# Optimization experiments

Hardware: AMD Instinct MI355X
Metric: run time of the kernel (lower is better)

The kernel has to match this reference:

```python
import jax, jax.numpy as jnp
import numpy as np

N_NODES = 50000
N_EDGES = 600000
F_IN = 128
HID = 128
LN_EPS = 1e-5


def setup_inputs() -> dict:
    key = jax.random.key(0)
    ks = jax.random.split(key, 8)
    x = jax.random.normal(ks[0], (N_NODES, F_IN), dtype=jnp.float32)
    edge_index = jax.random.randint(ks[1], (2, N_EDGES), 0, N_NODES, dtype=jnp.int64)
    s1 = 1.0 / np.sqrt(F_IN)
    s2 = 1.0 / np.sqrt(HID)
    return {
        "x": x,
        "edge_index": edge_index,
        "W1": jax.random.normal(ks[2], (F_IN, HID), dtype=jnp.float32) * s1,
        "b1": jnp.zeros((HID,), dtype=jnp.float32),
        "g1": jnp.ones((HID,), dtype=jnp.float32),
        "be1": jnp.zeros((HID,), dtype=jnp.float32),
        "W2": jax.random.normal(ks[3], (HID, HID), dtype=jnp.float32) * s2,
        "b2": jnp.zeros((HID,), dtype=jnp.float32),
        "g2": jnp.ones((HID,), dtype=jnp.float32),
        "be2": jnp.zeros((HID,), dtype=jnp.float32),
    }


def _layer_norm(h, g, b):
    mu = jnp.mean(h, axis=-1, keepdims=True)
    var = jnp.mean(jnp.square(h - mu), axis=-1, keepdims=True)
    return (h - mu) * jax.lax.rsqrt(var + LN_EPS) * g + b


def reference(x, edge_index, W1, b1, g1, be1, W2, b2, g2, be2):
    n = x.shape[0]
    src, dst = edge_index[0], edge_index[1]
    # GCN symmetric normalization with self-loops: deg = in-degree(A) + 1
    deg = jax.ops.segment_sum(jnp.ones_like(src, dtype=x.dtype), dst, num_segments=n) + 1.0
    dinv = jax.lax.rsqrt(deg)                       # D^{-1/2}, [N]
    enorm = (dinv[src] * dinv[dst])[:, None]        # per-edge norm, [E,1]
    self_norm = (dinv * dinv)[:, None]              # self-loop norm,  [N,1]

    def gcn(h, W, b):
        h = h @ W                                   # [N,HID]
        agg = jax.ops.segment_sum(h[src] * enorm, dst, num_segments=n)
        return agg + h * self_norm + b

    h = jax.nn.relu(_layer_norm(gcn(x, W1, b1), g1, be1))
    h = jax.nn.relu(_layer_norm(gcn(h, W2, b2), g2, be2))
    return h  # dropout is identity in eval; LSTM evolution only runs in training
```

## Files before the change

kernel.cpp:

```cpp
#include <hip/hip_runtime.h>

#define N_NODES 50000
#define N_EDGES 600000
#define HID 128
#define LN_EPS 1e-5f
#define MAXDEG 64
#define NB_GEMM1 782
#define NB_PLACE 2344

typedef __attribute__((ext_vector_type(8))) short short8;
typedef __attribute__((ext_vector_type(4))) float f32x4;

__device__ inline float b2f(unsigned short u) {
    union { unsigned int i; float f; } v;
    v.i = ((unsigned int)u) << 16;
    return v.f;
}
__device__ inline unsigned short f2b(float f) {
    union { float f; unsigned int u; } v; v.f = f;
    unsigned int r = (v.u + 0x7FFFu + ((v.u >> 16) & 1u)) >> 16;
    return (unsigned short)r;
}

__global__ __launch_bounds__(256) void k_fused1(const float* __restrict__ x,
                                                const float* __restrict__ W1,
                                                const float* __restrict__ W2,
                                                const int* __restrict__ ei,
                                                int* __restrict__ cursor,
                                                int* __restrict__ esrc,
                                                unsigned short* __restrict__ WT2,
                                                unsigned short* __restrict__ hb) {
    const int tid = threadIdx.x;

    if (blockIdx.x >= NB_GEMM1) {
        const int bi = blockIdx.x - NB_GEMM1;
        const int e = bi * 256 + tid;
        if (e < N_EDGES) {
            const int d = ei[N_EDGES + e];
            const int pos = atomicAdd(&cursor[d], 1);
            if (pos < MAXDEG) esrc[d * MAXDEG + pos] = ei[e];
        }
        if (bi < 64) {
            const int i = bi * 256 + tid;
            const int k = i >> 7, n = i & 127;
            WT2[n * 128 + k] = f2b(W2[i]);
        }
        return;
    }

    __shared__ unsigned short wt[16384];
    {
        const float4* W4 = (const float4*)W1;
#pragma unroll
        for (int it = 0; it < 16; ++it) {
            const int i4 = tid + 256 * it;
            const float4 v = W4[i4];
            const int k  = (i4 * 4) >> 7;
            const int n0 = (i4 * 4) & 127;
            wt[(n0 + 0) * 128 + (k ^ (((n0 + 0) & 7) << 3))] = f2b(v.x);
            wt[(n0 + 1) * 128 + (k ^ (((n0 + 1) & 7) << 3))] = f2b(v.y);
            wt[(n0 + 2) * 128 + (k ^ (((n0 + 2) & 7) << 3))] = f2b(v.z);
            wt[(n0 + 3) * 128 + (k ^ (((n0 + 3) & 7) << 3))] = f2b(v.w);
        }
    }
    __syncthreads();

    const int lane = tid & 63;
    const int ln   = lane & 15;
    const int quad = lane >> 4;
    const int m0   = blockIdx.x * 64 + (tid >> 6) * 16;

    f32x4 acc[8];
#pragma unroll
    for (int t = 0; t < 8; ++t) acc[t] = (f32x4){0.f, 0.f, 0.f, 0.f};

    int arow = m0 + ln;
    if (arow >= N_NODES) arow = N_NODES - 1;
    const float* aptr = x + (size_t)arow * HID + quad * 8;

#pragma unroll
    for (int ks = 0; ks < 4; ++ks) {
        const float4 v0 = *(const float4*)(aptr + ks * 32);
        const float4 v1 = *(const float4*)(aptr + ks * 32 + 4);
        short8 a;
        a[0] = (short)f2b(v0.x); a[1] = (short)f2b(v0.y);
        a[2] = (short)f2b(v0.z); a[3] = (short)f2b(v0.w);
        a[4] = (short)f2b(v1.x); a[5] = (short)f2b(v1.y);
        a[6] = (short)f2b(v1.z); a[7] = (short)f2b(v1.w);
#pragma unroll
        for (int t = 0; t < 8; ++t) {
            const int n = t * 16 + ln;
            const short8 b = *(const short8*)&wt[n * 128 + ((quad * 8 + ks * 32) ^ ((n & 7) << 3))];
            acc[t] = __builtin_amdgcn_mfma_f32_16x16x32_bf16(a, b, acc[t], 0, 0, 0);
        }
    }

#pragma unroll
    for (int t = 0; t < 8; ++t) {
#pragma unroll
        for (int r = 0; r < 4; ++r) {
            const int row = m0 + quad * 4 + r;
            if (row < N_NODES) hb[(size_t)row * HID + t * 16 + ln] = f2b(acc[t][r]);
        }
    }
}

template <bool FUSE>
__device__ __forceinline__ void agg_body(const int* __restrict__ cursor,
                                         const int* __restrict__ esrc,
                                         const unsigned short* __restrict__ h,
                                         const float* __restrict__ bia,
                                         const float* __restrict__ g,
                                         const float* __restrict__ be,
                                         const unsigned short* __restrict__ WT2,
                                         unsigned short* __restrict__ hb2,
                                         float* __restrict__ outf) {
    __shared__ float pbuf[2048];
    const int tid  = threadIdx.x;
    const int wv   = tid >> 6;
    const int lane = tid & 63;
    const int grp  = lane >> 4;
    const int fl   = lane & 15;
    const int half = wv >> 2;
    const int r    = (wv & 3) * 4 + grp;
    const int row  = blockIdx.x * 16 + r;

    const int cntA  = cursor[row];
    const int cnt   = cntA < MAXDEG ? cntA : MAXDEG;
    const int ebase = row * MAXDEG;
    const int c0    = ((cnt + 7) >> 3) << 2;
    const int h0n   = c0 < cnt ? c0 : cnt;
    const int eb    = half ? ebase + h0n : ebase;
    const int ee    = half ? ebase + cnt : ebase + h0n;

    float acc[8];
#pragma unroll
    for (int j = 0; j < 8; ++j) acc[j] = 0.f;

    int e = eb;
    for (; e + 3 < ee; e += 4) {
        const int4 s4 = *(const int4*)(esrc + e);
        const float w0 = rsqrtf((float)cursor[s4.x] + 1.0f);
        const float w1 = rsqrtf((float)cursor[s4.y] + 1.0f);
        const float w2 = rsqrtf((float)cursor[s4.z] + 1.0f);
        const float w3 = rsqrtf((float)cursor[s4.w] + 1.0f);
        const short8 v0 = *(const short8*)(h + (size_t)s4.x * HID + 8 * fl);
        const short8 v1 = *(const short8*)(h + (size_t)s4.y * HID + 8 * fl);
        const short8 v2 = *(const short8*)(h + (size_t)s4.z * HID + 8 * fl);
        const short8 v3 = *(const short8*)(h + (size_t)s4.w * HID + 8 * fl);
#pragma unroll
        for (int j = 0; j < 8; ++j) {
            acc[j] = fmaf(w0, b2f((unsigned short)v0[j]), acc[j]);
            acc[j] = fmaf(w1, b2f((unsigned short)v1[j]), acc[j]);
            acc[j] = fmaf(w2, b2f((unsigned short)v2[j]), acc[j]);
            acc[j] = fmaf(w3, b2f((unsigned short)v3[j]), acc[j]);
        }
    }
    for (; e < ee; ++e) {
        const int sA = esrc[e];
        const float wA = rsqrtf((float)cursor[sA] + 1.0f);
        const short8 vA = *(const short8*)(h + (size_t)sA * HID + 8 * fl);
#pragma unroll
        for (int j = 0; j < 8; ++j)
            acc[j] = fmaf(wA, b2f((unsigned short)vA[j]), acc[j]);
    }

    if (half == 1) {
#pragma unroll
        for (int j = 0; j < 8; ++j) pbuf[r * 128 + 8 * fl + j] = acc[j];
    }
    __syncthreads();

    float o[8];
    if (half == 0) {
#pragma unroll
        for (int j = 0; j < 8; ++j) acc[j] += pbuf[r * 128 + 8 * fl + j];

        const float dd = rsqrtf((float)cntA + 1.0f);
        const float sn = dd * dd;
        const short8 hv = *(const short8*)(h + (size_t)row * HID + 8 * fl);
        const float4 b0 = *(const float4*)(bia + 8 * fl);
        const float4 b1 = *(const float4*)(bia + 8 * fl + 4);
        const float bb[8] = {b0.x, b0.y, b0.z, b0.w, b1.x, b1.y, b1.z, b1.w};

        float v[8], s = 0.f, ss = 0.f;
#pragma unroll
        for (int j = 0; j < 8; ++j) {
            v[j] = dd * acc[j] + b2f((unsigned short)hv[j]) * sn + bb[j];
            s += v[j];
            ss = fmaf(v[j], v[j], ss);
        }
#pragma unroll
        for (int off = 1; off <= 8; off <<= 1) {
            s  += __shfl_xor(s, off);
            ss += __shfl_xor(ss, off);
        }
        const float mu  = s * (1.0f / 128.0f);
        const float var = ss * (1.0f / 128.0f) - mu * mu;
        const float rs  = rsqrtf(var + LN_EPS);

        const float4 g0  = *(const float4*)(g + 8 * fl);
        const float4 g1  = *(const float4*)(g + 8 * fl + 4);
        const float4 e0v = *(const float4*)(be + 8 * fl);
        const float4 e1v = *(const float4*)(be + 8 * fl + 4);
        const float gg[8] = {g0.x, g0.y, g0.z, g0.w, g1.x, g1.y, g1.z, g1.w};
        const float ee2[8] = {e0v.x, e0v.y, e0v.z, e0v.w, e1v.x, e1v.y, e1v.z, e1v.w};
#pragma unroll
        for (int j = 0; j < 8; ++j)
            o[j] = fmaxf((v[j] - mu) * rs * gg[j] + ee2[j], 0.0f);
    }

    if constexpr (!FUSE) {
        if (half == 0) {
            float4 w0 = {o[0], o[1], o[2], o[3]};
            float4 w1 = {o[4], o[5], o[6], o[7]};
            *(float4*)(outf + (size_t)row * HID + 8 * fl) = w0;
            *(float4*)(outf + (size_t)row * HID + 8 * fl + 4) = w1;
        }
    } else {
        __syncthreads();
        unsigned short* tile = (unsigned short*)pbuf;
        if (half == 0) {
            short8 w;
#pragma unroll
            for (int j = 0; j < 8; ++j) w[j] = (short)f2b(o[j]);
            *(short8*)&tile[r * 128 + ((8 * fl) ^ ((r & 7) << 3))] = w;
        }
        __syncthreads();

        f32x4 c = (f32x4){0.f, 0.f, 0.f, 0.f};
        const int n0 = wv * 16 + fl;
#pragma unroll
        for (int ks = 0; ks < 4; ++ks) {
            const short8 a  = *(const short8*)&tile[fl * 128 + ((grp * 8 + ks * 32) ^ ((fl & 7) << 3))];
            const short8 bf = *(const short8*)(WT2 + (size_t)n0 * HID + grp * 8 + ks * 32);
            c = __builtin_amdgcn_mfma_f32_16x16x32_bf16(a, bf, c, 0, 0, 0);
        }
#pragma unroll
        for (int rr = 0; rr < 4; ++rr) {
            const int orow = blockIdx.x * 16 + grp * 4 + rr;
            hb2[(size_t)orow * HID + n0] = f2b(c[rr]);
        }
    }
}

__global__ __launch_bounds__(512, 4) void k_agg_fuse(const int* __restrict__ cursor,
                                                     const int* __restrict__ esrc,
                                                     const unsigned short* __restrict__ h,
                                                     const float* __restrict__ bia,
                                                     const float* __restrict__ g,
                                                     const float* __restrict__ be,
                                                     const unsigned short* __restrict__ WT2,
                                                     unsigned short* __restrict__ hb2) {
    agg_body<true>(cursor, esrc, h, bia, g, be, WT2, hb2, nullptr);
}

__global__ __launch_bounds__(512, 4) void k_agg_out(const int* __restrict__ cursor,
                                                    const int* __restrict__ esrc,
                                                    const unsigned short* __restrict__ h,
                                                    const float* __restrict__ bia,
                                                    const float* __restrict__ g,
                                                    const float* __restrict__ be,
                                                    float* __restrict__ outf) {
    agg_body<false>(cursor, esrc, h, bia, g, be, nullptr, nullptr, outf);
}

extern "C" void kernel_launch(void* const* d_in, const int* in_sizes, int n_in,
                              void* d_out, int out_size, void* d_ws, size_t ws_size,
                              hipStream_t stream) {
    (void)in_sizes; (void)n_in; (void)out_size; (void)ws_size;

    const float* x   = (const float*)d_in[0];
    const int*   ei  = (const int*)d_in[1];
    const float* W1  = (const float*)d_in[2];
    const float* b1  = (const float*)d_in[3];
    const float* g1  = (const float*)d_in[4];
    const float* be1 = (const float*)d_in[5];
    const float* W2  = (const float*)d_in[6];
    const float* b2  = (const float*)d_in[7];
    const float* g2  = (const float*)d_in[8];
    const float* be2 = (const float*)d_in[9];
    float* out = (float*)d_out;

    int* cursor = (int*)d_ws;
    int* esrc   = (int*)d_ws + 50016;
    unsigned short* WT2 = (unsigned short*)((int*)d_ws + 3250016);
    unsigned short* hb  = (unsigned short*)((int*)d_ws + 3258208);
    unsigned short* hb2 = (unsigned short*)((int*)d_ws + 6458208);

    hipMemsetAsync(cursor, 0, N_NODES * sizeof(int), stream);
    k_fused1<<<NB_GEMM1 + NB_PLACE, 256, 0, stream>>>(x, W1, W2, ei, cursor, esrc, WT2, hb);

    k_agg_fuse<<<N_NODES / 16, 512, 0, stream>>>(cursor, esrc, hb, b1, g1, be1, WT2, hb2);
    k_agg_out<<<N_NODES / 16, 512, 0, stream>>>(cursor, esrc, hb2, b2, g2, be2, out);
}
```

Before: 188.7 us.

## Pre-scale layer-2 features by source degree norm and move weight transposes to prep kernel

The layer-1 fused kernel now multiplies its GEMM2 output rows by the source-node D^{-1/2}. This lets the second aggregation sum raw features without per-edge cursor lookups and rsqrt, and fold the self-loop and destination scaling into a single dd factor. Weight bf16 transposes and the cursor zeroing move into a small prep kernel that replaces the memset. The GEMM1 blocks now read B fragments directly from global WT1 instead of building a swizzled LDS copy per block. The trade is an extra launch plus uncoalesced-ish global B loads in GEMM1, in exchange for removing redundant per-block transpose work and gather traffic in the second aggregation.

```diff
diff --git a/kernel.cpp b/kernel.cpp
--- a/kernel.cpp
+++ b/kernel.cpp
@@ -22,48 +22,41 @@
     return (unsigned short)r;
 }
 
+__global__ __launch_bounds__(256) void k_prep(const float* __restrict__ W1,
+                                              const float* __restrict__ W2,
+                                              unsigned short* __restrict__ WT1,
+                                              unsigned short* __restrict__ WT2,
+                                              int* __restrict__ cursor) {
+    const int bid = blockIdx.x, tid = threadIdx.x;
+    if (bid < 64) {
+        const int i = bid * 256 + tid;
+        WT1[(i & 127) * 128 + (i >> 7)] = f2b(W1[i]);
+    } else if (bid < 128) {
+        const int i = (bid - 64) * 256 + tid;
+        WT2[(i & 127) * 128 + (i >> 7)] = f2b(W2[i]);
+    } else {
+        const int i = (bid - 128) * 256 + tid;
+        if (i < N_NODES) cursor[i] = 0;
+    }
+}
+
 __global__ __launch_bounds__(256) void k_fused1(const float* __restrict__ x,
-                                                const float* __restrict__ W1,
-                                                const float* __restrict__ W2,
+                                                const unsigned short* __restrict__ WT1,
                                                 const int* __restrict__ ei,
                                                 int* __restrict__ cursor,
                                                 int* __restrict__ esrc,
-                                                unsigned short* __restrict__ WT2,
                                                 unsigned short* __restrict__ hb) {
     const int tid = threadIdx.x;
 
     if (blockIdx.x >= NB_GEMM1) {
-        const int bi = blockIdx.x - NB_GEMM1;
-        const int e = bi * 256 + tid;
+        const int e = (blockIdx.x - NB_GEMM1) * 256 + tid;
         if (e < N_EDGES) {
             const int d = ei[N_EDGES + e];
             const int pos = atomicAdd(&cursor[d], 1);
             if (pos < MAXDEG) esrc[d * MAXDEG + pos] = ei[e];
         }
-        if (bi < 64) {
-            const int i = bi * 256 + tid;
-            const int k = i >> 7, n = i & 127;
-            WT2[n * 128 + k] = f2b(W2[i]);
-        }
         return;
     }
-
-    __shared__ unsigned short wt[16384];
-    {
-        const float4* W4 = (const float4*)W1;
-#pragma unroll
-        for (int it = 0; it < 16; ++it) {
-            const int i4 = tid + 256 * it;
-            const float4 v = W4[i4];
-            const int k  = (i4 * 4) >> 7;
-            const int n0 = (i4 * 4) & 127;
-            wt[(n0 + 0) * 128 + (k ^ (((n0 + 0) & 7) << 3))] = f2b(v.x);
-            wt[(n0 + 1) * 128 + (k ^ (((n0 + 1) & 7) << 3))] = f2b(v.y);
-            wt[(n0 + 2) * 128 + (k ^ (((n0 + 2) & 7) << 3))] = f2b(v.z);
-            wt[(n0 + 3) * 128 + (k ^ (((n0 + 3) & 7) << 3))] = f2b(v.w);
-        }
-    }
-    __syncthreads();
 
     const int lane = tid & 63;
     const int ln   = lane & 15;
@@ -77,6 +70,7 @@
     int arow = m0 + ln;
     if (arow >= N_NODES) arow = N_NODES - 1;
     const float* aptr = x + (size_t)arow * HID + quad * 8;
+    const unsigned short* bptr = WT1 + (size_t)ln * HID + quad * 8;
 
 #pragma unroll
     for (int ks = 0; ks < 4; ++ks) {
@@ -89,8 +83,7 @@
         a[6] = (short)f2b(v1.z); a[7] = (short)f2b(v1.w);
 #pragma unroll
         for (int t = 0; t < 8; ++t) {
-            const int n = t * 16 + ln;
-            const short8 b = *(const short8*)&wt[n * 128 + ((quad * 8 + ks * 32) ^ ((n & 7) << 3))];
+            const short8 b = *(const short8*)(bptr + (size_t)t * 16 * HID + ks * 32);
             acc[t] = __builtin_amdgcn_mfma_f32_16x16x32_bf16(a, b, acc[t], 0, 0, 0);
         }
     }
@@ -140,26 +133,35 @@
     int e = eb;
     for (; e + 3 < ee; e += 4) {
         const int4 s4 = *(const int4*)(esrc + e);
-        const float w0 = rsqrtf((float)cursor[s4.x] + 1.0f);
-        const float w1 = rsqrtf((float)cursor[s4.y] + 1.0f);
-        const float w2 = rsqrtf((float)cursor[s4.z] + 1.0f);
-        const float w3 = rsqrtf((float)cursor[s4.w] + 1.0f);
         const short8 v0 = *(const short8*)(h + (size_t)s4.x * HID + 8 * fl);
         const short8 v1 = *(const short8*)(h + (size_t)s4.y * HID + 8 * fl);
         const short8 v2 = *(const short8*)(h + (size_t)s4.z * HID + 8 * fl);
         const short8 v3 = *(const short8*)(h + (size_t)s4.w * HID + 8 * fl);
-#pragma unroll
-        for (int j = 0; j < 8; ++j) {
-            acc[j] = fmaf(w0, b2f((unsigned short)v0[j]), acc[j]);
-            acc[j] = fmaf(w1, b2f((unsigned short)v1[j]), acc[j]);
-            acc[j] = fmaf(w2, b2f((unsigned short)v2[j]), acc[j]);
-            acc[j] = fmaf(w3, b2f((unsigned short)v3[j]), acc[j]);
+        if constexpr (FUSE) {
+            const float w0 = rsqrtf((float)cursor[s4.x] + 1.0f);
+            const float w1 = rsqrtf((float)cursor[s4.y] + 1.0f);
+            const float w2 = rsqrtf((float)cursor[s4.z] + 1.0f);
+            const float w3 = rsqrtf((float)cursor[s4.w] + 1.0f);
+#pragma unroll
+            for (int j = 0; j < 8; ++j) {
+                acc[j] = fmaf(w0, b2f((unsigned short)v0[j]), acc[j]);
+                acc[j] = fmaf(w1, b2f((unsigned short)v1[j]), acc[j]);
+                acc[j] = fmaf(w2, b2f((unsigned short)v2[j]), acc[j]);
+                acc[j] = fmaf(w3, b2f((unsigned short)v3[j]), acc[j]);
+            }
+        } else {
+#pragma unroll
+            for (int j = 0; j < 8; ++j) {
+                acc[j] += b2f((unsigned short)v0[j]) + b2f((unsigned short)v1[j]);
+                acc[j] += b2f((unsigned short)v2[j]) + b2f((unsigned short)v3[j]);
+            }
         }
     }
     for (; e < ee; ++e) {
         const int sA = esrc[e];
-        const float wA = rsqrtf((float)cursor[sA] + 1.0f);
         const short8 vA = *(const short8*)(h + (size_t)sA * HID + 8 * fl);
+        float wA = 1.0f;
+        if constexpr (FUSE) wA = rsqrtf((float)cursor[sA] + 1.0f);
 #pragma unroll
         for (int j = 0; j < 8; ++j)
             acc[j] = fmaf(wA, b2f((unsigned short)vA[j]), acc[j]);
@@ -177,7 +179,6 @@
         for (int j = 0; j < 8; ++j) acc[j] += pbuf[r * 128 + 8 * fl + j];
 
         const float dd = rsqrtf((float)cntA + 1.0f);
-        const float sn = dd * dd;
         const short8 hv = *(const short8*)(h + (size_t)row * HID + 8 * fl);
         const float4 b0 = *(const float4*)(bia + 8 * fl);
         const float4 b1 = *(const float4*)(bia + 8 * fl + 4);
@@ -186,7 +187,12 @@
         float v[8], s = 0.f, ss = 0.f;
 #pragma unroll
         for (int j = 0; j < 8; ++j) {
-            v[j] = dd * acc[j] + b2f((unsigned short)hv[j]) * sn + bb[j];
+            if constexpr (FUSE) {
+                const float sn = dd * dd;
+                v[j] = dd * acc[j] + b2f((unsigned short)hv[j]) * sn + bb[j];
+            } else {
+                v[j] = dd * (acc[j] + b2f((unsigned short)hv[j])) + bb[j];
+            }
             s += v[j];
             ss = fmaf(v[j], v[j], ss);
         }
@@ -239,7 +245,8 @@
 #pragma unroll
         for (int rr = 0; rr < 4; ++rr) {
             const int orow = blockIdx.x * 16 + grp * 4 + rr;
-            hb2[(size_t)orow * HID + n0] = f2b(c[rr]);
+            const float sc = rsqrtf((float)cursor[orow] + 1.0f);
+            hb2[(size_t)orow * HID + n0] = f2b(c[rr] * sc);
         }
     }
 }
@@ -284,12 +291,13 @@
 
     int* cursor = (int*)d_ws;
     int* esrc   = (int*)d_ws + 50016;
-    unsigned short* WT2 = (unsigned short*)((int*)d_ws + 3250016);
-    unsigned short* hb  = (unsigned short*)((int*)d_ws + 3258208);
-    unsigned short* hb2 = (unsigned short*)((int*)d_ws + 6458208);
-
-    hipMemsetAsync(cursor, 0, N_NODES * sizeof(int), stream);
-    k_fused1<<<NB_GEMM1 + NB_PLACE, 256, 0, stream>>>(x, W1, W2, ei, cursor, esrc, WT2, hb);
+    unsigned short* WT1 = (unsigned short*)((int*)d_ws + 3250016);
+    unsigned short* WT2 = (unsigned short*)((int*)d_ws + 3258208);
+    unsigned short* hb  = (unsigned short*)((int*)d_ws + 3266400);
+    unsigned short* hb2 = (unsigned short*)((int*)d_ws + 6466400);
+
+    k_prep<<<324, 256, 0, stream>>>(W1, W2, WT1, WT2, cursor);
+    k_fused1<<<NB_GEMM1 + NB_PLACE, 256, 0, stream>>>(x, WT1, ei, cursor, esrc, hb);
 
     k_agg_fuse<<<N_NODES / 16, 512, 0, stream>>>(cursor, esrc, hb, b1, g1, be1, WT2, hb2);
     k_agg_out<<<N_NODES / 16, 512, 0, stream>>>(cursor, esrc, hb2, b2, g2, be2, out);
```

Result: slower. 213.8 us (+13.3%).

## Prescale layer-2 features by source norm and persist GEMM1 blocks

Applied to the files above, without the earlier changes.

The layer-2 GEMM output is now prescaled by each node's D^{-1/2}. The second aggregation can then sum neighbor rows unweighted, without gathering each source's degree, and the self term folds into one multiply. Separately, the first GEMM now runs as 160 persistent blocks looping over 782 row tiles. This amortizes the per-block bf16 W1 staging into shared memory and leaves more slots for the edge-placement blocks. The prescaling removes a random cursor load and rsqrt per edge, at the cost of an extra rounding of the scaled values into bf16.

```diff
diff --git a/kernel.cpp b/kernel.cpp
--- a/kernel.cpp
+++ b/kernel.cpp
@@ -5,7 +5,8 @@
 #define HID 128
 #define LN_EPS 1e-5f
 #define MAXDEG 64
-#define NB_GEMM1 782
+#define NT_GEMM 782
+#define NB_GEMM 160
 #define NB_PLACE 2344
 
 typedef __attribute__((ext_vector_type(8))) short short8;
@@ -32,8 +33,8 @@
                                                 unsigned short* __restrict__ hb) {
     const int tid = threadIdx.x;
 
-    if (blockIdx.x >= NB_GEMM1) {
-        const int bi = blockIdx.x - NB_GEMM1;
+    if (blockIdx.x >= NB_GEMM) {
+        const int bi = blockIdx.x - NB_GEMM;
         const int e = bi * 256 + tid;
         if (e < N_EDGES) {
             const int d = ei[N_EDGES + e];
@@ -42,8 +43,7 @@
         }
         if (bi < 64) {
             const int i = bi * 256 + tid;
-            const int k = i >> 7, n = i & 127;
-            WT2[n * 128 + k] = f2b(W2[i]);
+            WT2[(i & 127) * 128 + (i >> 7)] = f2b(W2[i]);
         }
         return;
     }
@@ -68,39 +68,42 @@
     const int lane = tid & 63;
     const int ln   = lane & 15;
     const int quad = lane >> 4;
-    const int m0   = blockIdx.x * 64 + (tid >> 6) * 16;
-
-    f32x4 acc[8];
-#pragma unroll
-    for (int t = 0; t < 8; ++t) acc[t] = (f32x4){0.f, 0.f, 0.f, 0.f};
-
-    int arow = m0 + ln;
-    if (arow >= N_NODES) arow = N_NODES - 1;
-    const float* aptr = x + (size_t)arow * HID + quad * 8;
-
-#pragma unroll
-    for (int ks = 0; ks < 4; ++ks) {
-        const float4 v0 = *(const float4*)(aptr + ks * 32);
-        const float4 v1 = *(const float4*)(aptr + ks * 32 + 4);
-        short8 a;
-        a[0] = (short)f2b(v0.x); a[1] = (short)f2b(v0.y);
-        a[2] = (short)f2b(v0.z); a[3] = (short)f2b(v0.w);
-        a[4] = (short)f2b(v1.x); a[5] = (short)f2b(v1.y);
-        a[6] = (short)f2b(v1.z); a[7] = (short)f2b(v1.w);
+
+    for (int mt = blockIdx.x; mt < NT_GEMM; mt += NB_GEMM) {
+        const int m0 = mt * 64 + (tid >> 6) * 16;
+
+        f32x4 acc[8];
+#pragma unroll
+        for (int t = 0; t < 8; ++t) acc[t] = (f32x4){0.f, 0.f, 0.f, 0.f};
+
+        int arow = m0 + ln;
+        if (arow >= N_NODES) arow = N_NODES - 1;
+        const float* aptr = x + (size_t)arow * HID + quad * 8;
+
+#pragma unroll
+        for (int ks = 0; ks < 4; ++ks) {
+            const float4 v0 = *(const float4*)(aptr + ks * 32);
+            const float4 v1 = *(const float4*)(aptr + ks * 32 + 4);
+            short8 a;
+            a[0] = (short)f2b(v0.x); a[1] = (short)f2b(v0.y);
+            a[2] = (short)f2b(v0.z); a[3] = (short)f2b(v0.w);
+            a[4] = (short)f2b(v1.x); a[5] = (short)f2b(v1.y);
+            a[6] = (short)f2b(v1.z); a[7] = (short)f2b(v1.w);
+#pragma unroll
+            for (int t = 0; t < 8; ++t) {
+                const int n = t * 16 + ln;
+                const short8 b = *(const short8*)&wt[n * 128 + ((quad * 8 + ks * 32) ^ ((n & 7) << 3))];
+                acc[t] = __builtin_amdgcn_mfma_f32_16x16x32_bf16(a, b, acc[t], 0, 0, 0);
+            }
+        }
+
 #pragma unroll
         for (int t = 0; t < 8; ++t) {
-            const int n = t * 16 + ln;
-            const short8 b = *(const short8*)&wt[n * 128 + ((quad * 8 + ks * 32) ^ ((n & 7) << 3))];
-            acc[t] = __builtin_amdgcn_mfma_f32_16x16x32_bf16(a, b, acc[t], 0, 0, 0);
-        }
-    }
-
-#pragma unroll
-    for (int t = 0; t < 8; ++t) {
-#pragma unroll
-        for (int r = 0; r < 4; ++r) {
-            const int row = m0 + quad * 4 + r;
-            if (row < N_NODES) hb[(size_t)row * HID + t * 16 + ln] = f2b(acc[t][r]);
+#pragma unroll
+            for (int r = 0; r < 4; ++r) {
+                const int row = m0 + quad * 4 + r;
+                if (row < N_NODES) hb[(size_t)row * HID + t * 16 + ln] = f2b(acc[t][r]);
+            }
         }
     }
 }
@@ -140,26 +143,35 @@
     int e = eb;
     for (; e + 3 < ee; e += 4) {
         const int4 s4 = *(const int4*)(esrc + e);
-        const float w0 = rsqrtf((float)cursor[s4.x] + 1.0f);
-        const float w1 = rsqrtf((float)cursor[s4.y] + 1.0f);
-        const float w2 = rsqrtf((float)cursor[s4.z] + 1.0f);
-        const float w3 = rsqrtf((float)cursor[s4.w] + 1.0f);
         const short8 v0 = *(const short8*)(h + (size_t)s4.x * HID + 8 * fl);
         const short8 v1 = *(const short8*)(h + (size_t)s4.y * HID + 8 * fl);
         const short8 v2 = *(const short8*)(h + (size_t)s4.z * HID + 8 * fl);
         const short8 v3 = *(const short8*)(h + (size_t)s4.w * HID + 8 * fl);
-#pragma unroll
-        for (int j = 0; j < 8; ++j) {
-            acc[j] = fmaf(w0, b2f((unsigned short)v0[j]), acc[j]);
-            acc[j] = fmaf(w1, b2f((unsigned short)v1[j]), acc[j]);
-            acc[j] = fmaf(w2, b2f((unsigned short)v2[j]), acc[j]);
-            acc[j] = fmaf(w3, b2f((unsigned short)v3[j]), acc[j]);
+        if constexpr (FUSE) {
+            const float w0 = rsqrtf((float)cursor[s4.x] + 1.0f);
+            const float w1 = rsqrtf((float)cursor[s4.y] + 1.0f);
+            const float w2 = rsqrtf((float)cursor[s4.z] + 1.0f);
+            const float w3 = rsqrtf((float)cursor[s4.w] + 1.0f);
+#pragma unroll
+            for (int j = 0; j < 8; ++j) {
+                acc[j] = fmaf(w0, b2f((unsigned short)v0[j]), acc[j]);
+                acc[j] = fmaf(w1, b2f((unsigned short)v1[j]), acc[j]);
+                acc[j] = fmaf(w2, b2f((unsigned short)v2[j]), acc[j]);
+                acc[j] = fmaf(w3, b2f((unsigned short)v3[j]), acc[j]);
+            }
+        } else {
+#pragma unroll
+            for (int j = 0; j < 8; ++j) {
+                acc[j] += b2f((unsigned short)v0[j]) + b2f((unsigned short)v1[j]);
+                acc[j] += b2f((unsigned short)v2[j]) + b2f((unsigned short)v3[j]);
+            }
         }
     }
     for (; e < ee; ++e) {
         const int sA = esrc[e];
-        const float wA = rsqrtf((float)cursor[sA] + 1.0f);
         const short8 vA = *(const short8*)(h + (size_t)sA * HID + 8 * fl);
+        float wA = 1.0f;
+        if constexpr (FUSE) wA = rsqrtf((float)cursor[sA] + 1.0f);
 #pragma unroll
         for (int j = 0; j < 8; ++j)
             acc[j] = fmaf(wA, b2f((unsigned short)vA[j]), acc[j]);
@@ -177,7 +189,6 @@
         for (int j = 0; j < 8; ++j) acc[j] += pbuf[r * 128 + 8 * fl + j];
 
         const float dd = rsqrtf((float)cntA + 1.0f);
-        const float sn = dd * dd;
         const short8 hv = *(const short8*)(h + (size_t)row * HID + 8 * fl);
         const float4 b0 = *(const float4*)(bia + 8 * fl);
         const float4 b1 = *(const float4*)(bia + 8 * fl + 4);
@@ -186,7 +197,12 @@
         float v[8], s = 0.f, ss = 0.f;
 #pragma unroll
         for (int j = 0; j < 8; ++j) {
-            v[j] = dd * acc[j] + b2f((unsigned short)hv[j]) * sn + bb[j];
+            if constexpr (FUSE) {
+                const float sn = dd * dd;
+                v[j] = dd * acc[j] + b2f((unsigned short)hv[j]) * sn + bb[j];
+            } else {
+                v[j] = dd * (acc[j] + b2f((unsigned short)hv[j])) + bb[j];
+            }
             s += v[j];
             ss = fmaf(v[j], v[j], ss);
         }
@@ -239,7 +255,8 @@
 #pragma unroll
         for (int rr = 0; rr < 4; ++rr) {
             const int orow = blockIdx.x * 16 + grp * 4 + rr;
-            hb2[(size_t)orow * HID + n0] = f2b(c[rr]);
+            const float sc = rsqrtf((float)cursor[orow] + 1.0f);
+            hb2[(size_t)orow * HID + n0] = f2b(c[rr] * sc);
         }
     }
 }
@@ -289,7 +306,7 @@
     unsigned short* hb2 = (unsigned short*)((int*)d_ws + 6458208);
 
     hipMemsetAsync(cursor, 0, N_NODES * sizeof(int), stream);
-    k_fused1<<<NB_GEMM1 + NB_PLACE, 256, 0, stream>>>(x, W1, W2, ei, cursor, esrc, WT2, hb);
+    k_fused1<<<NB_GEMM + NB_PLACE, 256, 0, stream>>>(x, W1, W2, ei, cursor, esrc, WT2, hb);
 
     k_agg_fuse<<<N_NODES / 16, 512, 0, stream>>>(cursor, esrc, hb, b1, g1, be1, WT2, hb2);
     k_agg_out<<<N_NODES / 16, 512, 0, stream>>>(cursor, esrc, hb2, b2, g2, be2, out);
```

After: 193.4 us. +2.5%, slower.
